# Performance work log

Hardware: AMD Instinct MI355X
Metric: run time of the kernel (lower is better)

The kernel has to match this reference:

```python
import jax, jax.numpy as jnp
import numpy as np

EPS = 1e-6

def setup_inputs() -> dict:
    key = jax.random.key(0)
    k1, k2, k3 = jax.random.split(key, 3)
    N, L, S, H, D = 4, 4096, 4096, 8, 64
    queries = jax.random.normal(k1, (N, L, H, D), dtype=jnp.float32)
    keys = jax.random.normal(k2, (N, S, H, D), dtype=jnp.float32)
    values = jax.random.normal(k3, (N, S, H, D), dtype=jnp.float32)
    return {"queries": queries, "keys": keys, "values": values}

def _feature_map(x):
    # elu(x) + 1
    return jax.nn.elu(x) + 1.0

def reference(queries, keys, values):
    Q = _feature_map(queries)          # [N, L, H, D]
    K = _feature_map(keys)             # [N, S, H, D]
    v_length = values.shape[1]
    v = values / v_length              # [N, S, H, Dv]
    # KV outer-product sum over source positions: [N, H, D, Dv]
    KV = jnp.einsum('nshd,nshv->nhdv', K, v)
    # Normalizer: Q . sum_s K  -> [N, L, H]
    Z = 1.0 / (jnp.einsum('nlhd,nhd->nlh', Q, K.sum(axis=1)) + EPS)
    # Queried values: [N, L, H, Dv]
    out = jnp.einsum('nlhd,nhdv,nlh->nlhv', Q, KV, Z) * v_length
    return out
```

## Files before the change

kernel.cpp:

```cpp
#include <hip/hip_runtime.h>

#define NB   4
#define LQ   4096
#define SK   4096
#define NHD  8
#define DD   64
#define ROWSTRIDE (NHD * DD)
#define CH   16
#define SROWS (SK / CH)
#define TS   16
#define KVSZ (DD * DD)
#define PART_STRIDE (KVSZ + DD)
#define NHTOT (NB * NHD)
#define LT   64
#define EPSF 1e-6f

__device__ __forceinline__ float fmap(float x) {
    return x > 0.f ? x + 1.f : __expf(x);
}

__global__ __launch_bounds__(256) void k1_kv(const float* __restrict__ Kin,
                                             const float* __restrict__ Vin,
                                             float* __restrict__ part) {
    const int blk   = blockIdx.x;
    const int nh    = blk / CH;
    const int chunk = blk % CH;
    const int n = nh / NHD, h = nh % NHD;
    const int t = threadIdx.x;
    const int r  = t >> 4;
    const int c  = (t & 15) << 2;
    const int d0 = c;
    const int e0 = r << 2;

    __shared__ __align__(16) float Ks[TS][DD];
    __shared__ __align__(16) float Vs[TS][DD];
    __shared__ __align__(16) float ksred[TS][DD];

    float acc[4][4] = {};
    float ksl[4] = {0.f, 0.f, 0.f, 0.f};

    const size_t base = ((size_t)n * SK + (size_t)chunk * SROWS) * ROWSTRIDE
                        + (size_t)h * DD;

    for (int s0 = 0; s0 < SROWS; s0 += TS) {
        const size_t g = base + (size_t)(s0 + r) * ROWSTRIDE + c;
        float4 kg = *(const float4*)(Kin + g);
        float4 vg = *(const float4*)(Vin + g);
        float4 kf;
        kf.x = fmap(kg.x); kf.y = fmap(kg.y); kf.z = fmap(kg.z); kf.w = fmap(kg.w);
        ksl[0] += kf.x; ksl[1] += kf.y; ksl[2] += kf.z; ksl[3] += kf.w;
        __syncthreads();
        *(float4*)&Ks[r][c] = kf;
        *(float4*)&Vs[r][c] = vg;
        __syncthreads();
#pragma unroll
        for (int s = 0; s < TS; ++s) {
            float4 k4 = *(float4*)&Ks[s][d0];
            float4 v4 = *(float4*)&Vs[s][e0];
            float kk[4] = {k4.x, k4.y, k4.z, k4.w};
            float vv[4] = {v4.x, v4.y, v4.z, v4.w};
#pragma unroll
            for (int i = 0; i < 4; ++i)
#pragma unroll
                for (int j = 0; j < 4; ++j)
                    acc[i][j] += kk[i] * vv[j];
        }
    }

    __syncthreads();
    *(float4*)&ksred[r][c] = make_float4(ksl[0], ksl[1], ksl[2], ksl[3]);
    __syncthreads();

    float* pb = part + ((size_t)nh * CH + chunk) * PART_STRIDE;
    if (t < DD) {
        float s = 0.f;
#pragma unroll
        for (int rr = 0; rr < TS; ++rr) s += ksred[rr][t];
        pb[KVSZ + t] = s;
    }
#pragma unroll
    for (int i = 0; i < 4; ++i) {
        float4 o = make_float4(acc[i][0], acc[i][1], acc[i][2], acc[i][3]);
        *(float4*)(pb + (d0 + i) * DD + e0) = o;
    }
}

__global__ __launch_bounds__(256) void k2_reduce(const float* __restrict__ part,
                                                 float* __restrict__ fin) {
    const int idx = blockIdx.x * 256 + threadIdx.x;
    if (idx >= NHTOT * PART_STRIDE) return;
    const int nh = idx / PART_STRIDE;
    const int j  = idx - nh * PART_STRIDE;
    const float* p = part + (size_t)nh * CH * PART_STRIDE + j;
    float s = 0.f;
#pragma unroll
    for (int cix = 0; cix < CH; ++cix) s += p[(size_t)cix * PART_STRIDE];
    fin[idx] = s;
}

#define QPAD 68
__global__ __launch_bounds__(256) void k3_out(const float* __restrict__ Qin,
                                              const float* __restrict__ fin,
                                              float* __restrict__ out) {
    const int blk = blockIdx.x;
    const int nh  = blk >> 6;
    const int lc  = blk & 63;
    const int n = nh >> 3, h = nh & 7;
    const int t = threadIdx.x;

    __shared__ __align__(16) float KVs[DD][DD];
    __shared__ __align__(16) float Ksm[DD];
    __shared__ __align__(16) float Qs[LT][QPAD];

    const float* fb = fin + (size_t)nh * PART_STRIDE;
    float* kvflat = &KVs[0][0];
    for (int i = t * 4; i < KVSZ; i += 1024)
        *(float4*)(kvflat + i) = *(const float4*)(fb + i);
    if (t < DD) Ksm[t] = fb[KVSZ + t];

    const int r = t >> 4;
    const int c = (t & 15) << 2;
    const size_t qbase = ((size_t)n * LQ + (size_t)lc * LT) * ROWSTRIDE
                         + (size_t)h * DD;
    for (int rr = r; rr < LT; rr += 16) {
        float4 q = *(const float4*)(Qin + qbase + (size_t)rr * ROWSTRIDE + c);
        float4 qf;
        qf.x = fmap(q.x); qf.y = fmap(q.y); qf.z = fmap(q.z); qf.w = fmap(q.w);
        *(float4*)&Qs[rr][c] = qf;
    }
    __syncthreads();

    const int e0 = (t & 15) << 2;
    const int l0 = (t >> 4) << 2;
    float acc[4][4] = {};
    float z[4] = {0.f, 0.f, 0.f, 0.f};

#pragma unroll 4
    for (int d0 = 0; d0 < DD; d0 += 4) {
        float4 km4 = *(float4*)&Ksm[d0];
        float km[4] = {km4.x, km4.y, km4.z, km4.w};
        float q[4][4];
        float kv[4][4];
#pragma unroll
        for (int i = 0; i < 4; ++i) {
            float4 q4 = *(float4*)&Qs[l0 + i][d0];
            q[i][0] = q4.x; q[i][1] = q4.y; q[i][2] = q4.z; q[i][3] = q4.w;
        }
#pragma unroll
        for (int s = 0; s < 4; ++s) {
            float4 kv4 = *(float4*)&KVs[d0 + s][e0];
            kv[s][0] = kv4.x; kv[s][1] = kv4.y; kv[s][2] = kv4.z; kv[s][3] = kv4.w;
        }
#pragma unroll
        for (int i = 0; i < 4; ++i)
#pragma unroll
            for (int s = 0; s < 4; ++s) {
                z[i] += q[i][s] * km[s];
#pragma unroll
                for (int j = 0; j < 4; ++j)
                    acc[i][j] += q[i][s] * kv[s][j];
            }
    }

#pragma unroll
    for (int i = 0; i < 4; ++i) {
        float zi = 1.f / (z[i] + EPSF);
        float4 o = make_float4(acc[i][0] * zi, acc[i][1] * zi,
                               acc[i][2] * zi, acc[i][3] * zi);
        *(float4*)(out + ((size_t)n * LQ + (size_t)lc * LT + l0 + i) * ROWSTRIDE
                   + (size_t)h * DD + e0) = o;
    }
}

extern "C" void kernel_launch(void* const* d_in, const int* in_sizes, int n_in,
                              void* d_out, int out_size, void* d_ws, size_t ws_size,
                              hipStream_t stream) {
    const float* Q = (const float*)d_in[0];
    const float* K = (const float*)d_in[1];
    const float* V = (const float*)d_in[2];
    float* out = (float*)d_out;

    float* ws   = (float*)d_ws;
    float* part = ws;
    float* fin  = ws + (size_t)NHTOT * CH * PART_STRIDE;

    k1_kv<<<NHTOT * CH, 256, 0, stream>>>(K, V, part);
    k2_reduce<<<(NHTOT * PART_STRIDE + 255) / 256, 256, 0, stream>>>(part, fin);
    k3_out<<<NHTOT * (LQ / LT), 256, 0, stream>>>(Q, fin, out);
}
```

Baseline: 164.5 us.

## Use split-bf16 MFMA for KV accumulation and output projection

Both the KV outer-product kernel and the output kernel now use bf16 MFMA 16x16x32 instructions instead of scalar FP32 FMAs. Each FP32 operand is split into hi and lo bf16 parts and three MFMAs are issued to keep close to FP32 accuracy. The output kernel stages KV transposed into swizzled bf16 shared memory and loads Q directly from global into registers, dropping the Q shared tile. In exchange, k1 now does scalar strided global loads instead of float4, and the dropped lo*lo term adds a small precision risk.

Measured after the change: 142.1 us (median of 2 runs). 1.16x faster.

```diff
diff --git a/kernel.cpp b/kernel.cpp
--- a/kernel.cpp
+++ b/kernel.cpp
@@ -1,4 +1,5 @@
 #include <hip/hip_runtime.h>
+#include <stdint.h>
 
 #define NB   4
 #define LQ   4096
@@ -8,15 +9,33 @@
 #define ROWSTRIDE (NHD * DD)
 #define CH   16
 #define SROWS (SK / CH)
-#define TS   16
 #define KVSZ (DD * DD)
 #define PART_STRIDE (KVSZ + DD)
 #define NHTOT (NB * NHD)
 #define LT   64
 #define EPSF 1e-6f
 
+typedef __attribute__((ext_vector_type(8))) short bf16x8;
+typedef __attribute__((ext_vector_type(4))) float f32x4;
+
+union FragU { uint32_t u[4]; bf16x8 v; };
+
 __device__ __forceinline__ float fmap(float x) {
     return x > 0.f ? x + 1.f : __expf(x);
+}
+
+__device__ __forceinline__ void split8(const float* x, bf16x8& hi, bf16x8& lo) {
+    FragU H, L;
+#pragma unroll
+    for (int p = 0; p < 4; ++p) {
+        float a = x[2*p], b = x[2*p+1];
+        uint32_t ua = __float_as_uint(a), ub = __float_as_uint(b);
+        float ra = a - __uint_as_float(ua & 0xFFFF0000u);
+        float rb = b - __uint_as_float(ub & 0xFFFF0000u);
+        H.u[p] = (ua >> 16) | (ub & 0xFFFF0000u);
+        L.u[p] = (__float_as_uint(ra) >> 16) | (__float_as_uint(rb) & 0xFFFF0000u);
+    }
+    hi = H.v; lo = L.v;
 }
 
 __global__ __launch_bounds__(256) void k1_kv(const float* __restrict__ Kin,
@@ -27,61 +46,76 @@
     const int chunk = blk % CH;
     const int n = nh / NHD, h = nh % NHD;
     const int t = threadIdx.x;
-    const int r  = t >> 4;
-    const int c  = (t & 15) << 2;
-    const int d0 = c;
-    const int e0 = r << 2;
-
-    __shared__ __align__(16) float Ks[TS][DD];
-    __shared__ __align__(16) float Vs[TS][DD];
-    __shared__ __align__(16) float ksred[TS][DD];
-
-    float acc[4][4] = {};
-    float ksl[4] = {0.f, 0.f, 0.f, 0.f};
+    const int w = t >> 6, lane = t & 63;
+    const int g = lane >> 4, r = lane & 15;
+    const int wm = w & 1, wn = w >> 1;
 
     const size_t base = ((size_t)n * SK + (size_t)chunk * SROWS) * ROWSTRIDE
                         + (size_t)h * DD;
 
-    for (int s0 = 0; s0 < SROWS; s0 += TS) {
-        const size_t g = base + (size_t)(s0 + r) * ROWSTRIDE + c;
-        float4 kg = *(const float4*)(Kin + g);
-        float4 vg = *(const float4*)(Vin + g);
-        float4 kf;
-        kf.x = fmap(kg.x); kf.y = fmap(kg.y); kf.z = fmap(kg.z); kf.w = fmap(kg.w);
-        ksl[0] += kf.x; ksl[1] += kf.y; ksl[2] += kf.z; ksl[3] += kf.w;
-        __syncthreads();
-        *(float4*)&Ks[r][c] = kf;
-        *(float4*)&Vs[r][c] = vg;
-        __syncthreads();
-#pragma unroll
-        for (int s = 0; s < TS; ++s) {
-            float4 k4 = *(float4*)&Ks[s][d0];
-            float4 v4 = *(float4*)&Vs[s][e0];
-            float kk[4] = {k4.x, k4.y, k4.z, k4.w};
-            float vv[4] = {v4.x, v4.y, v4.z, v4.w};
-#pragma unroll
-            for (int i = 0; i < 4; ++i)
-#pragma unroll
-                for (int j = 0; j < 4; ++j)
-                    acc[i][j] += kk[i] * vv[j];
-        }
-    }
-
-    __syncthreads();
-    *(float4*)&ksred[r][c] = make_float4(ksl[0], ksl[1], ksl[2], ksl[3]);
-    __syncthreads();
+    const f32x4 zero4 = {0.f, 0.f, 0.f, 0.f};
+    f32x4 acc[2][2] = {{zero4, zero4}, {zero4, zero4}};
+    float ks[2] = {0.f, 0.f};
+
+    for (int s0 = 0; s0 < SROWS; s0 += 32) {
+        float xa[2][8], xb[2][8];
+#pragma unroll
+        for (int i = 0; i < 8; ++i) {
+            const int soff = ((i & 4) << 2) + 4 * g + (i & 3);
+            const size_t rowb = base + (size_t)(s0 + soff) * ROWSTRIDE;
+#pragma unroll
+            for (int mt = 0; mt < 2; ++mt)
+                xa[mt][i] = Kin[rowb + (wm*2 + mt)*16 + r];
+#pragma unroll
+            for (int nt = 0; nt < 2; ++nt)
+                xb[nt][i] = Vin[rowb + (wn*2 + nt)*16 + r];
+        }
+        bf16x8 ahi[2], alo[2], bhi[2], blo[2];
+#pragma unroll
+        for (int mt = 0; mt < 2; ++mt) {
+#pragma unroll
+            for (int i = 0; i < 8; ++i) xa[mt][i] = fmap(xa[mt][i]);
+            if (wn == 0) {
+#pragma unroll
+                for (int i = 0; i < 8; ++i) ks[mt] += xa[mt][i];
+            }
+            split8(xa[mt], ahi[mt], alo[mt]);
+        }
+#pragma unroll
+        for (int nt = 0; nt < 2; ++nt) split8(xb[nt], bhi[nt], blo[nt]);
+#pragma unroll
+        for (int mt = 0; mt < 2; ++mt)
+#pragma unroll
+            for (int nt = 0; nt < 2; ++nt) {
+                acc[mt][nt] = __builtin_amdgcn_mfma_f32_16x16x32_bf16(
+                                  ahi[mt], bhi[nt], acc[mt][nt], 0, 0, 0);
+                acc[mt][nt] = __builtin_amdgcn_mfma_f32_16x16x32_bf16(
+                                  alo[mt], bhi[nt], acc[mt][nt], 0, 0, 0);
+                acc[mt][nt] = __builtin_amdgcn_mfma_f32_16x16x32_bf16(
+                                  ahi[mt], blo[nt], acc[mt][nt], 0, 0, 0);
+            }
+    }
 
     float* pb = part + ((size_t)nh * CH + chunk) * PART_STRIDE;
-    if (t < DD) {
-        float s = 0.f;
-#pragma unroll
-        for (int rr = 0; rr < TS; ++rr) s += ksred[rr][t];
-        pb[KVSZ + t] = s;
-    }
-#pragma unroll
-    for (int i = 0; i < 4; ++i) {
-        float4 o = make_float4(acc[i][0], acc[i][1], acc[i][2], acc[i][3]);
-        *(float4*)(pb + (d0 + i) * DD + e0) = o;
+#pragma unroll
+    for (int mt = 0; mt < 2; ++mt) {
+        const int dbase = (wm*2 + mt)*16 + 4*g;
+#pragma unroll
+        for (int nt = 0; nt < 2; ++nt) {
+            const int e = (wn*2 + nt)*16 + r;
+#pragma unroll
+            for (int j = 0; j < 4; ++j)
+                pb[(dbase + j) * DD + e] = acc[mt][nt][j];
+        }
+    }
+    if (wn == 0) {
+#pragma unroll
+        for (int mt = 0; mt < 2; ++mt) {
+            float v = ks[mt];
+            v += __shfl_xor(v, 16);
+            v += __shfl_xor(v, 32);
+            if (lane < 16) pb[KVSZ + (wm*2 + mt)*16 + lane] = v;
+        }
     }
 }
 
@@ -98,7 +132,8 @@
     fin[idx] = s;
 }
 
-#define QPAD 68
+#define KVSTR 72
+
 __global__ __launch_bounds__(256) void k3_out(const float* __restrict__ Qin,
                                               const float* __restrict__ fin,
                                               float* __restrict__ out) {
@@ -107,68 +142,77 @@
     const int lc  = blk & 63;
     const int n = nh >> 3, h = nh & 7;
     const int t = threadIdx.x;
-
-    __shared__ __align__(16) float KVs[DD][DD];
+    const int w = t >> 6, lane = t & 63;
+    const int g = lane >> 4, r = lane & 15;
+
+    __shared__ __align__(16) short KThi[DD][KVSTR];
+    __shared__ __align__(16) short KTlo[DD][KVSTR];
     __shared__ __align__(16) float Ksm[DD];
-    __shared__ __align__(16) float Qs[LT][QPAD];
 
     const float* fb = fin + (size_t)nh * PART_STRIDE;
-    float* kvflat = &KVs[0][0];
-    for (int i = t * 4; i < KVSZ; i += 1024)
-        *(float4*)(kvflat + i) = *(const float4*)(fb + i);
-    if (t < DD) Ksm[t] = fb[KVSZ + t];
-
-    const int r = t >> 4;
-    const int c = (t & 15) << 2;
-    const size_t qbase = ((size_t)n * LQ + (size_t)lc * LT) * ROWSTRIDE
-                         + (size_t)h * DD;
-    for (int rr = r; rr < LT; rr += 16) {
-        float4 q = *(const float4*)(Qin + qbase + (size_t)rr * ROWSTRIDE + c);
-        float4 qf;
-        qf.x = fmap(q.x); qf.y = fmap(q.y); qf.z = fmap(q.z); qf.w = fmap(q.w);
-        *(float4*)&Qs[rr][c] = qf;
+    {
+        const int e  = t & 63;
+        const int dq = t >> 6;
+#pragma unroll
+        for (int dd = 0; dd < 16; ++dd) {
+            const int d = dq * 16 + dd;
+            const float x = fb[d * DD + e];
+            const int col = (((d & 32) | (d & 3) | (((d >> 4) & 1) << 2)
+                              | (((d >> 2) & 3) << 3)) ^ ((e & 3) << 3));
+            const uint32_t ux = __float_as_uint(x);
+            const float lo = x - __uint_as_float(ux & 0xFFFF0000u);
+            KThi[e][col] = (short)(ux >> 16);
+            KTlo[e][col] = (short)(__float_as_uint(lo) >> 16);
+        }
+        if (t < DD) Ksm[t] = fb[KVSZ + t];
     }
     __syncthreads();
 
-    const int e0 = (t & 15) << 2;
-    const int l0 = (t >> 4) << 2;
-    float acc[4][4] = {};
-    float z[4] = {0.f, 0.f, 0.f, 0.f};
-
-#pragma unroll 4
-    for (int d0 = 0; d0 < DD; d0 += 4) {
-        float4 km4 = *(float4*)&Ksm[d0];
-        float km[4] = {km4.x, km4.y, km4.z, km4.w};
-        float q[4][4];
-        float kv[4][4];
-#pragma unroll
-        for (int i = 0; i < 4; ++i) {
-            float4 q4 = *(float4*)&Qs[l0 + i][d0];
-            q[i][0] = q4.x; q[i][1] = q4.y; q[i][2] = q4.z; q[i][3] = q4.w;
-        }
-#pragma unroll
-        for (int s = 0; s < 4; ++s) {
-            float4 kv4 = *(float4*)&KVs[d0 + s][e0];
-            kv[s][0] = kv4.x; kv[s][1] = kv4.y; kv[s][2] = kv4.z; kv[s][3] = kv4.w;
-        }
-#pragma unroll
-        for (int i = 0; i < 4; ++i)
-#pragma unroll
-            for (int s = 0; s < 4; ++s) {
-                z[i] += q[i][s] * km[s];
-#pragma unroll
-                for (int j = 0; j < 4; ++j)
-                    acc[i][j] += q[i][s] * kv[s][j];
-            }
-    }
-
-#pragma unroll
-    for (int i = 0; i < 4; ++i) {
-        float zi = 1.f / (z[i] + EPSF);
-        float4 o = make_float4(acc[i][0] * zi, acc[i][1] * zi,
-                               acc[i][2] * zi, acc[i][3] * zi);
-        *(float4*)(out + ((size_t)n * LQ + (size_t)lc * LT + l0 + i) * ROWSTRIDE
-                   + (size_t)h * DD + e0) = o;
+    const size_t qrow = (size_t)n * LQ + (size_t)lc * LT + w * 16 + r;
+    const float* qp = Qin + qrow * ROWSTRIDE + (size_t)h * DD;
+
+    const f32x4 zero4 = {0.f, 0.f, 0.f, 0.f};
+    f32x4 acc[4] = {zero4, zero4, zero4, zero4};
+    float z = 0.f;
+
+#pragma unroll
+    for (int kst = 0; kst < 2; ++kst) {
+        const int kb = kst * 32;
+        const float4 qa = *(const float4*)(qp + kb + 4*g);
+        const float4 qb = *(const float4*)(qp + kb + 16 + 4*g);
+        float qv[8] = {fmap(qa.x), fmap(qa.y), fmap(qa.z), fmap(qa.w),
+                       fmap(qb.x), fmap(qb.y), fmap(qb.z), fmap(qb.w)};
+        const float4 ka = *(const float4*)&Ksm[kb + 4*g];
+        const float4 kc = *(const float4*)&Ksm[kb + 16 + 4*g];
+        z += qv[0]*ka.x + qv[1]*ka.y + qv[2]*ka.z + qv[3]*ka.w
+           + qv[4]*kc.x + qv[5]*kc.y + qv[6]*kc.z + qv[7]*kc.w;
+        bf16x8 ahi, alo;
+        split8(qv, ahi, alo);
+        const int cswz = 8 * (g ^ (r & 3));
+#pragma unroll
+        for (int nt = 0; nt < 4; ++nt) {
+            const int e = nt*16 + r;
+            const bf16x8 bh = *(const bf16x8*)&KThi[e][kb + cswz];
+            const bf16x8 bl = *(const bf16x8*)&KTlo[e][kb + cswz];
+            acc[nt] = __builtin_amdgcn_mfma_f32_16x16x32_bf16(ahi, bh, acc[nt], 0,0,0);
+            acc[nt] = __builtin_amdgcn_mfma_f32_16x16x32_bf16(alo, bh, acc[nt], 0,0,0);
+            acc[nt] = __builtin_amdgcn_mfma_f32_16x16x32_bf16(ahi, bl, acc[nt], 0,0,0);
+        }
+    }
+
+    z += __shfl_xor(z, 16);
+    z += __shfl_xor(z, 32);
+
+    const size_t obase0 = ((size_t)n * LQ + (size_t)lc * LT + w * 16) * ROWSTRIDE
+                          + (size_t)h * DD;
+#pragma unroll
+    for (int j = 0; j < 4; ++j) {
+        const float zj = __shfl(z, 4*g + j);
+        const float zi = 1.f / (zj + EPSF);
+        const size_t ob = obase0 + (size_t)(4*g + j) * ROWSTRIDE;
+#pragma unroll
+        for (int nt = 0; nt < 4; ++nt)
+            out[ob + nt*16 + r] = acc[nt][j] * zi;
     }
 }
 
```
